# Kernel optimization log

Measured on AMD Instinct MI355X. Metric: run time of the kernel, lower is better.

The kernel has to match this reference:

```python
import jax, jax.numpy as jnp
import numpy as np

N_NODES = 50000
N_EDGES = 800000
D_IN = 128
D_OUT = 128
N_MLP = 2


def _lin(x, W, b):
    return x @ W.T + b


def setup_inputs() -> dict:
    key = jax.random.key(0)
    ks = jax.random.split(key, 32)
    d = {}
    d['feat'] = jax.random.normal(ks[0], (N_NODES, D_IN), dtype=jnp.float32)
    d['src'] = jax.random.randint(ks[1], (N_EDGES,), 0, N_NODES, dtype=jnp.int32)
    d['dst'] = jax.random.randint(ks[2], (N_EDGES,), 0, N_NODES, dtype=jnp.int32)
    s_in = 1.0 / np.sqrt(D_IN)
    s_out = 1.0 / np.sqrt(D_OUT)
    i = 3
    def w(shape, s):
        nonlocal i
        out = jax.random.normal(ks[i], shape, dtype=jnp.float32) * s
        i += 1
        return out
    for nm in ['asrc', 'adst', 'asub', 'amul']:
        d['W_' + nm] = w((D_OUT, D_IN), s_in)
        d['b_' + nm] = w((D_OUT,), s_in)
    d['W_aout'] = w((1, D_OUT), s_out)
    d['b_aout'] = w((1,), s_out)
    for nm in ['pool', 'pool2']:
        d['W_' + nm] = w((D_IN, D_IN), s_in)
        d['b_' + nm] = w((D_IN,), s_in)
    for nm in ['self', 'neigh', 'neigh2']:
        d['W_' + nm] = w((D_OUT, D_IN), s_in)
        d['b_' + nm] = w((D_OUT,), s_in)
    d['W_mlp'] = w((N_MLP, D_OUT, D_OUT), s_out)
    d['b_mlp'] = w((N_MLP, D_OUT), s_out)
    return d


def reference(feat, src, dst,
              W_asrc, b_asrc, W_adst, b_adst, W_asub, b_asub, W_amul, b_amul,
              W_aout, b_aout, W_pool, b_pool, W_pool2, b_pool2,
              W_self, b_self, W_neigh, b_neigh, W_neigh2, b_neigh2,
              W_mlp, b_mlp):
    gelu = lambda x: jax.nn.gelu(x, approximate=False)
    fs = feat[src]            # [E, D_IN] gathered source feats
    fd = feat[dst]            # [E, D_IN] gathered dest feats
    # edge attention score
    e = _lin(fs - fd, W_asub, b_asub) + _lin(fs * fd, W_amul, b_amul)
    e = e + _lin(feat, W_asrc, b_asrc)[src] + _lin(feat, W_adst, b_adst)[dst]
    e = gelu(e)
    e = jax.nn.leaky_relu(_lin(e, W_aout, b_aout), 0.2)  # [E, 1]
    deg = jax.ops.segment_sum(jnp.ones((src.shape[0],), jnp.float32), dst,
                              num_segments=N_NODES)      # in-degree
    has_in = (deg > 0)[:, None]
    # max-pool branch
    h = gelu(_lin(feat, W_pool, b_pool))
    m = e * h[src]
    neigh = jax.ops.segment_max(m, dst, num_segments=N_NODES)
    neigh = jnp.where(has_in, neigh, 0.0)
    # mean-pool branch
    h2 = gelu(_lin(feat, W_pool2, b_pool2))
    m2 = e * h2[src]
    neigh2 = jax.ops.segment_sum(m2, dst, num_segments=N_NODES)
    neigh2 = neigh2 / jnp.maximum(deg, 1.0)[:, None]
    rst = _lin(feat, W_self, b_self) + _lin(neigh, W_neigh, b_neigh) \
        + _lin(neigh2, W_neigh2, b_neigh2)
    for li in range(W_mlp.shape[0]):
        rst = rst + _lin(gelu(rst), W_mlp[li], b_mlp[li])
    return rst
```

## Files before the change

kernel.cpp:

```cpp
#include <hip/hip_runtime.h>
#include <cstdint>
#include <cstddef>

#define NN 50000
#define NE 800000
#define DD 128

static_assert(NN % 16 == 0, "node tiles");
static_assert(NE % 16 == 0, "edge tiles");

typedef __bf16 bf16_t;
typedef bf16_t bf16x8 __attribute__((ext_vector_type(8)));
typedef bf16_t bf16x4 __attribute__((ext_vector_type(4)));
typedef bf16_t bf16x2 __attribute__((ext_vector_type(2)));
typedef float f32x4 __attribute__((ext_vector_type(4)));
typedef float f32x16 __attribute__((ext_vector_type(16)));

__device__ __forceinline__ float gelu_f(float x) {
    float u = x * x;
    float t = fmaf(u, -0.1029442445f, -2.3021184019f);
    float s = __builtin_amdgcn_exp2f(x * t);
    return x * __builtin_amdgcn_rcpf(1.0f + s);
}

__device__ __forceinline__ int frag_idx(int ch, int k) {
    int t = ch >> 4, n = ch & 15;
    int kb = k >> 5, r = k & 31, q = r >> 3, j = r & 7;
    return ((((t * 4 + kb) * 4 + q) * 16 + n) << 3) + j;
}

__device__ __forceinline__ int frag32_idx(int ch, int k) {
    int t = ch >> 5, m = ch & 31;
    int kc = k >> 4, q = (k >> 3) & 1, j = k & 7;
    return ((((t * 8 + kc) * 2 + q) * 32 + m) << 3) + j;
}

__global__ __launch_bounds__(256) void convert_feat_kernel(
    const float* __restrict__ feat, bf16_t* __restrict__ fb,
    const int* __restrict__ dst, int* __restrict__ deg)
{
    int i = blockIdx.x * 256 + threadIdx.x;
    f32x4 v = ((const f32x4*)feat)[i];
    bf16x4 o;
    o[0] = (bf16_t)v[0]; o[1] = (bf16_t)v[1]; o[2] = (bf16_t)v[2]; o[3] = (bf16_t)v[3];
    ((bf16x4*)fb)[i] = o;
    if (i < NE) atomicAdd(&deg[dst[i]], 1);
}

__global__ __launch_bounds__(256) void prep_kernel(
    const float* __restrict__ W_asrc, const float* __restrict__ b_asrc,
    const float* __restrict__ W_adst, const float* __restrict__ b_adst,
    const float* __restrict__ W_asub, const float* __restrict__ b_asub,
    const float* __restrict__ W_amul, const float* __restrict__ b_amul,
    const float* __restrict__ W_pool, const float* __restrict__ W_pool2,
    const float* __restrict__ W_self, const float* __restrict__ b_self,
    const float* __restrict__ W_neigh, const float* __restrict__ b_neigh,
    const float* __restrict__ W_neigh2, const float* __restrict__ b_neigh2,
    const float* __restrict__ W_mlp,
    bf16_t* __restrict__ W_Sf, bf16_t* __restrict__ W_Df, bf16_t* __restrict__ W_amulf,
    bf16_t* __restrict__ W_poolf, bf16_t* __restrict__ W_pool2f,
    bf16_t* __restrict__ W_selff, bf16_t* __restrict__ W_neighf, bf16_t* __restrict__ W_neigh2f,
    bf16_t* __restrict__ W_mlpf,
    float* __restrict__ b_e, float* __restrict__ b_rst)
{
    int gid = blockIdx.x * 256 + threadIdx.x;
    float sub = W_asub[gid];
    int ch = gid >> 7, k = gid & 127;
    int fi = frag_idx(ch, k);
    W_Sf[fi] = (bf16_t)(W_asrc[gid] + sub);
    W_Df[fi] = (bf16_t)(W_adst[gid] - sub);
    W_amulf[frag32_idx(ch, k)] = (bf16_t)W_amul[gid];
    W_poolf[fi]   = (bf16_t)W_pool[gid];
    W_pool2f[fi]  = (bf16_t)W_pool2[gid];
    W_selff[fi]   = (bf16_t)W_self[gid];
    W_neighf[fi]  = (bf16_t)W_neigh[gid];
    W_neigh2f[fi] = (bf16_t)W_neigh2[gid];
    W_mlpf[fi]            = (bf16_t)W_mlp[gid];
    W_mlpf[DD * DD + fi]  = (bf16_t)W_mlp[DD * DD + gid];
    if (gid < DD) {
        b_e[gid]   = b_asub[gid] + b_amul[gid] + b_asrc[gid] + b_adst[gid];
        b_rst[gid] = b_self[gid] + b_neigh[gid] + b_neigh2[gid];
    }
}

__device__ __forceinline__ void mm16_store_ilv(
    const bf16x8 a[4], const bf16_t* __restrict__ Wf, const float* __restrict__ bias,
    bf16_t* __restrict__ hh, int nb, int n, int q, int lane, int sub)
{
#pragma unroll
    for (int t = 0; t < 8; t++) {
        f32x4 acc = {0.f, 0.f, 0.f, 0.f};
#pragma unroll
        for (int kb = 0; kb < 4; kb++) {
            bf16x8 b = *(const bf16x8*)(Wf + (((t * 4 + kb) * 64 + lane) << 3));
            acc = __builtin_amdgcn_mfma_f32_16x16x32_bf16(a[kb], b, acc, 0, 0, 0);
        }
        int ch = t * 16 + n;
        int pos = ((ch >> 1) << 2) + (ch & 1) + sub;
        float bv = bias[ch];
#pragma unroll
        for (int r = 0; r < 4; r++)
            hh[(size_t)(nb + q * 4 + r) * 256 + pos] = (bf16_t)gelu_f(acc[r] + bv);
    }
}

__device__ __forceinline__ void mm16_store_plain(
    const bf16x8 a[4], const bf16_t* __restrict__ Wf, const float* __restrict__ bias,
    bf16_t* __restrict__ out, int nb, int n, int q, int lane)
{
#pragma unroll
    for (int t = 0; t < 8; t++) {
        f32x4 acc = {0.f, 0.f, 0.f, 0.f};
#pragma unroll
        for (int kb = 0; kb < 4; kb++) {
            bf16x8 b = *(const bf16x8*)(Wf + (((t * 4 + kb) * 64 + lane) << 3));
            acc = __builtin_amdgcn_mfma_f32_16x16x32_bf16(a[kb], b, acc, 0, 0, 0);
        }
        int ch = t * 16 + n;
        float bv = bias ? bias[ch] : 0.0f;
#pragma unroll
        for (int r = 0; r < 4; r++)
            out[(size_t)(nb + q * 4 + r) * DD + ch] = (bf16_t)(acc[r] + bv);
    }
}

__global__ __launch_bounds__(256) void node_linear_kernel(
    const bf16_t* __restrict__ fb,
    const bf16_t* __restrict__ W_poolf, const float* __restrict__ b_pool,
    const bf16_t* __restrict__ W_pool2f, const float* __restrict__ b_pool2,
    const bf16_t* __restrict__ W_Sf, const float* __restrict__ b_e,
    const bf16_t* __restrict__ W_Df,
    const int* __restrict__ src, const int* __restrict__ dst,
    int* __restrict__ cursor, int2* __restrict__ csr,
    bf16_t* __restrict__ hh, bf16_t* __restrict__ us, bf16_t* __restrict__ ud)
{
    int gtid = blockIdx.x * 256 + threadIdx.x;
    if (gtid < NE / 4) {
        int4 s4 = ((const int4*)src)[gtid];
        int4 d4 = ((const int4*)dst)[gtid];
#pragma unroll
        for (int j = 0; j < 4; j++) {
            int d = (&d4.x)[j];
            int pos = atomicAdd(&cursor[d << 4], 1);
            int2 pk;
            pk.x = (&s4.x)[j];
            pk.y = d;
            csr[pos] = pk;
        }
    }

    int wid = blockIdx.x * 4 + (threadIdx.x >> 6);
    if (wid >= NN / 16) return;
    int lane = threadIdx.x & 63, n = lane & 15, q = lane >> 4;
    int nb = wid * 16;
    bf16x8 a[4];
#pragma unroll
    for (int kb = 0; kb < 4; kb++)
        a[kb] = *(const bf16x8*)(fb + (size_t)(nb + n) * DD + kb * 32 + q * 8);
    mm16_store_ilv(a, W_poolf, b_pool, hh, nb, n, q, lane, 0);
    mm16_store_ilv(a, W_pool2f, b_pool2, hh, nb, n, q, lane, 2);
    mm16_store_plain(a, W_Sf, b_e, us, nb, n, q, lane);
    mm16_store_plain(a, W_Df, nullptr, ud, nb, n, q, lane);
}

#define SCAN_NB ((NN + 255) / 256)

__global__ __launch_bounds__(256) void scan1_kernel(const int* __restrict__ deg,
                                                    int* __restrict__ offsets, int* __restrict__ bsum)
{
    __shared__ int tmp[256];
    int t = threadIdx.x, g = blockIdx.x * 256 + t;
    int v = (g < NN) ? deg[g] : 0;
    tmp[t] = v;
    __syncthreads();
#pragma unroll
    for (int d = 1; d < 256; d <<= 1) {
        int x = (t >= d) ? tmp[t - d] : 0;
        __syncthreads();
        tmp[t] += x;
        __syncthreads();
    }
    if (g < NN) offsets[g] = tmp[t] - v;
    if (t == 255) bsum[blockIdx.x] = tmp[255];
}

__global__ __launch_bounds__(256) void scan2_kernel(const int* __restrict__ bsum, int* __restrict__ bbase)
{
    __shared__ int tmp[256];
    int t = threadIdx.x;
    int v = (t < SCAN_NB) ? bsum[t] : 0;
    tmp[t] = v;
    __syncthreads();
#pragma unroll
    for (int d = 1; d < 256; d <<= 1) {
        int x = (t >= d) ? tmp[t - d] : 0;
        __syncthreads();
        tmp[t] += x;
        __syncthreads();
    }
    if (t < SCAN_NB) bbase[t] = tmp[t] - v;
}

__global__ __launch_bounds__(256) void scan3_kernel(const int* __restrict__ bbase,
                                                    int* __restrict__ offsets, int* __restrict__ cursor)
{
    int g = blockIdx.x * 256 + threadIdx.x;
    if (g < NN) {
        int o = offsets[g] + bbase[blockIdx.x];
        offsets[g] = o;
        cursor[g << 4] = o;
    }
}

#define ES_NBLK 2500
#define ES_ITERS (NE / 32 / ES_NBLK)

__global__ __launch_bounds__(256, 4) void edge_score_kernel(
    const bf16_t* __restrict__ fb,
    const bf16_t* __restrict__ us, const bf16_t* __restrict__ ud,
    const bf16_t* __restrict__ W_amulf,
    const float* __restrict__ w_aout, const float* __restrict__ b_aout,
    int2* __restrict__ csr)
{
    __shared__ __align__(16) bf16_t sP[2][32 * 128];
    __shared__ __align__(16) bf16_t sU[2][32 * 128];
    __shared__ float partials[32 * 5];
    __shared__ float sWa[128];
    int tid = threadIdx.x;
    int wave = tid >> 6, lane = tid & 63;
    int n = lane & 31, q = lane >> 5;
    int t = wave;

    if (tid < 128) sWa[tid] = w_aout[tid];

    bf16x8 wAm[8];
#pragma unroll
    for (int kc = 0; kc < 8; kc++)
        wAm[kc] = *(const bf16x8*)(W_amulf + ((((t * 8 + kc) * 2 + q) * 32 + n) << 3));
    float bout = b_aout[0];

    int sed0 = tid >> 4, sc = tid & 15;

    int e0 = blockIdx.x * 32;
    int2 pk0 = csr[e0 + sed0];
    int2 pk1 = csr[e0 + sed0 + 16];
    bf16x8 pfs0 = *(const bf16x8*)(fb + (size_t)pk0.x * DD + sc * 8);
    bf16x8 pfd0 = *(const bf16x8*)(fb + (size_t)pk0.y * DD + sc * 8);
    bf16x8 pus0 = *(const bf16x8*)(us + (size_t)pk0.x * DD + sc * 8);
    bf16x8 pud0 = *(const bf16x8*)(ud + (size_t)pk0.y * DD + sc * 8);
    bf16x8 pfs1 = *(const bf16x8*)(fb + (size_t)pk1.x * DD + sc * 8);
    bf16x8 pfd1 = *(const bf16x8*)(fb + (size_t)pk1.y * DD + sc * 8);
    bf16x8 pus1 = *(const bf16x8*)(us + (size_t)pk1.x * DD + sc * 8);
    bf16x8 pud1 = *(const bf16x8*)(ud + (size_t)pk1.y * DD + sc * 8);

    for (int it = 0; it < ES_ITERS; it++) {
        int buf = it & 1;
        int eb = (blockIdx.x + it * ES_NBLK) * 32;
        {
            bf16x8 pp, uu;
#pragma unroll
            for (int j = 0; j < 8; j++) {
                pp[j] = (bf16_t)((float)pfs0[j] * (float)pfd0[j]);
                uu[j] = (bf16_t)((float)pus0[j] + (float)pud0[j]);
            }
            int ph = (sc ^ (sed0 & 7)) << 3;
            *(bf16x8*)(sP[buf] + sed0 * 128 + ph) = pp;
            *(bf16x8*)(sU[buf] + sed0 * 128 + ph) = uu;
        }
        {
            int ed = sed0 + 16;
            bf16x8 pp, uu;
#pragma unroll
            for (int j = 0; j < 8; j++) {
                pp[j] = (bf16_t)((float)pfs1[j] * (float)pfd1[j]);
                uu[j] = (bf16_t)((float)pus1[j] + (float)pud1[j]);
            }
            int ph = (sc ^ (ed & 7)) << 3;
            *(bf16x8*)(sP[buf] + ed * 128 + ph) = pp;
            *(bf16x8*)(sU[buf] + ed * 128 + ph) = uu;
        }
        __syncthreads();
        if (it + 1 < ES_ITERS) {
            int e1 = (blockIdx.x + (it + 1) * ES_NBLK) * 32;
            pk0 = csr[e1 + sed0];
            pk1 = csr[e1 + sed0 + 16];
            pfs0 = *(const bf16x8*)(fb + (size_t)pk0.x * DD + sc * 8);
            pfd0 = *(const bf16x8*)(fb + (size_t)pk0.y * DD + sc * 8);
            pus0 = *(const bf16x8*)(us + (size_t)pk0.x * DD + sc * 8);
            pud0 = *(const bf16x8*)(ud + (size_t)pk0.y * DD + sc * 8);
            pfs1 = *(const bf16x8*)(fb + (size_t)pk1.x * DD + sc * 8);
            pfd1 = *(const bf16x8*)(fb + (size_t)pk1.y * DD + sc * 8);
            pus1 = *(const bf16x8*)(us + (size_t)pk1.x * DD + sc * 8);
            pud1 = *(const bf16x8*)(ud + (size_t)pk1.y * DD + sc * 8);
        }
        f32x16 acc = {};
        int swz = n & 7;
#pragma unroll
        for (int kc = 0; kc < 8; kc++) {
            bf16x8 bP = *(const bf16x8*)(sP[buf] + n * 128 + (((kc * 2 + q) ^ swz) << 3));
            acc = __builtin_amdgcn_mfma_f32_32x32x16_bf16(wAm[kc], bP, acc, 0, 0, 0);
        }
        float psum = 0.f;
#pragma unroll
        for (int c = 0; c < 4; c++) {
            bf16x4 sv = *(const bf16x4*)(sU[buf] + n * 128 + (((t * 4 + c) ^ swz) << 3) + q * 4);
            f32x4 wv = *(const f32x4*)(sWa + t * 32 + c * 8 + q * 4);
#pragma unroll
            for (int j = 0; j < 4; j++)
                psum = fmaf(gelu_f(acc[c * 4 + j] + (float)sv[j]), wv[j], psum);
        }
        psum += __shfl_xor(psum, 32, 64);
        if (lane < 32) partials[lane * 5 + wave] = psum;
        __syncthreads();
        if (wave == (it & 3) && lane < 32) {
            const float* pr = partials + lane * 5;
            float s = pr[0] + pr[1] + pr[2] + pr[3] + bout;
            s = s > 0.f ? s : 0.2f * s;
            csr[eb + lane].y = __float_as_int(s);
        }
    }
}

__global__ __launch_bounds__(256) void aggregate_kernel(
    const bf16_t* __restrict__ hh,
    const int* __restrict__ offsets, const int* __restrict__ deg,
    const int2* __restrict__ csr,
    bf16_t* __restrict__ neigh, bf16_t* __restrict__ neigh2)
{
    int wave = threadIdx.x >> 6, lane = threadIdx.x & 63;
    int v = blockIdx.x * 4 + wave;
    if (v >= NN) return;
    int off = offsets[v];
    int dg = deg[v];
    int quarter = lane >> 4;
    int cl = lane & 15;
    float mx[8], sm[8];
#pragma unroll
    for (int j = 0; j < 8; j++) { mx[j] = -INFINITY; sm[j] = 0.f; }
    for (int base = 0; base < dg; base += 64) {
        int cnt = dg - base; if (cnt > 64) cnt = 64;
        int s_l = 0; float sc_l = 0.f;
        if (lane < cnt) {
            int2 pk = csr[off + base + lane];
            s_l = pk.x;
            sc_l = __int_as_float(pk.y);
        }
        int nit = (cnt + 3) >> 2;
#pragma unroll 2
        for (int i = 0; i < nit; i++) {
            int idx = 4 * i + quarter;
            int s = __shfl(s_l, idx, 64);
            float sc = __shfl(sc_l, idx, 64);
            if (idx < cnt) {
                const bf16_t* row = hh + (size_t)s * 256 + 16 * cl;
                bf16x8 h0 = *(const bf16x8*)(row);
                bf16x8 h1 = *(const bf16x8*)(row + 8);
                mx[0] = fmaxf(mx[0], sc * (float)h0[0]);
                mx[1] = fmaxf(mx[1], sc * (float)h0[1]);
                sm[0] = fmaf(sc, (float)h0[2], sm[0]);
                sm[1] = fmaf(sc, (float)h0[3], sm[1]);
                mx[2] = fmaxf(mx[2], sc * (float)h0[4]);
                mx[3] = fmaxf(mx[3], sc * (float)h0[5]);
                sm[2] = fmaf(sc, (float)h0[6], sm[2]);
                sm[3] = fmaf(sc, (float)h0[7], sm[3]);
                mx[4] = fmaxf(mx[4], sc * (float)h1[0]);
                mx[5] = fmaxf(mx[5], sc * (float)h1[1]);
                sm[4] = fmaf(sc, (float)h1[2], sm[4]);
                sm[5] = fmaf(sc, (float)h1[3], sm[5]);
                mx[6] = fmaxf(mx[6], sc * (float)h1[4]);
                mx[7] = fmaxf(mx[7], sc * (float)h1[5]);
                sm[6] = fmaf(sc, (float)h1[6], sm[6]);
                sm[7] = fmaf(sc, (float)h1[7], sm[7]);
            }
        }
    }
#pragma unroll
    for (int j = 0; j < 8; j++) {
        mx[j] = fmaxf(mx[j], __shfl_xor(mx[j], 16, 64));
        mx[j] = fmaxf(mx[j], __shfl_xor(mx[j], 32, 64));
        sm[j] += __shfl_xor(sm[j], 16, 64);
        sm[j] += __shfl_xor(sm[j], 32, 64);
    }
    if (quarter == 0) {
        float inv = 1.0f / (float)(dg > 1 ? dg : 1);
        bf16x8 n1, n2;
#pragma unroll
        for (int j = 0; j < 8; j++) {
            n1[j] = (bf16_t)(dg > 0 ? mx[j] : 0.0f);
            n2[j] = (bf16_t)(sm[j] * inv);
        }
        *(bf16x8*)(neigh + (size_t)v * DD + 8 * cl) = n1;
        *(bf16x8*)(neigh2 + (size_t)v * DD + 8 * cl) = n2;
    }
}

__global__ __launch_bounds__(256) void final_kernel(
    const bf16_t* __restrict__ fb, const bf16_t* __restrict__ neigh, const bf16_t* __restrict__ neigh2,
    const bf16_t* __restrict__ W_selff, const bf16_t* __restrict__ W_neighf, const bf16_t* __restrict__ W_neigh2f,
    const float* __restrict__ b_rst,
    const bf16_t* __restrict__ W_mlpf, const float* __restrict__ b_mlp,
    float* __restrict__ out)
{
    __shared__ __align__(16) float lds[4][16 * 132];
    int wave = threadIdx.x >> 6;
    int wid = blockIdx.x * 4 + wave;
    if (wid >= NN / 16) return;
    int lane = threadIdx.x & 63, n = lane & 15, q = lane >> 4;
    int nb = wid * 16;
    float* L = lds[wave];

    bf16x8 af[4], an[4], am[4];
#pragma unroll
    for (int kb = 0; kb < 4; kb++) {
        size_t o = (size_t)(nb + n) * DD + kb * 32 + q * 8;
        af[kb] = *(const bf16x8*)(fb + o);
        an[kb] = *(const bf16x8*)(neigh + o);
        am[kb] = *(const bf16x8*)(neigh2 + o);
    }
    f32x4 rst[8];
#pragma unroll
    for (int t = 0; t < 8; t++) {
        f32x4 acc = {0.f, 0.f, 0.f, 0.f};
#pragma unroll
        for (int kb = 0; kb < 4; kb++) {
            int wo = ((t * 4 + kb) * 64 + lane) << 3;
            acc = __builtin_amdgcn_mfma_f32_16x16x32_bf16(af[kb], *(const bf16x8*)(W_selff + wo), acc, 0, 0, 0);
            acc = __builtin_amdgcn_mfma_f32_16x16x32_bf16(an[kb], *(const bf16x8*)(W_neighf + wo), acc, 0, 0, 0);
            acc = __builtin_amdgcn_mfma_f32_16x16x32_bf16(am[kb], *(const bf16x8*)(W_neigh2f + wo), acc, 0, 0, 0);
        }
        float bv = b_rst[t * 16 + n];
#pragma unroll
        for (int r = 0; r < 4; r++) acc[r] += bv;
        rst[t] = acc;
    }

#pragma unroll
    for (int li = 0; li < 2; li++) {
#pragma unroll
        for (int t = 0; t < 8; t++)
#pragma unroll
            for (int r = 0; r < 4; r++)
                L[(q * 4 + r) * 132 + t * 16 + n] = gelu_f(rst[t][r]);
        __builtin_amdgcn_wave_barrier();
        bf16x8 g[4];
#pragma unroll
        for (int kb = 0; kb < 4; kb++) {
            const f32x4* p = (const f32x4*)&L[n * 132 + kb * 32 + q * 8];
            f32x4 x0 = p[0], x1 = p[1];
            bf16x8 gg;
            gg[0] = (bf16_t)x0[0]; gg[1] = (bf16_t)x0[1]; gg[2] = (bf16_t)x0[2]; gg[3] = (bf16_t)x0[3];
            gg[4] = (bf16_t)x1[0]; gg[5] = (bf16_t)x1[1]; gg[6] = (bf16_t)x1[2]; gg[7] = (bf16_t)x1[3];
            g[kb] = gg;
        }
        __builtin_amdgcn_wave_barrier();
        const bf16_t* Wl = W_mlpf + li * DD * DD;
#pragma unroll
        for (int t = 0; t < 8; t++) {
            f32x4 acc = {0.f, 0.f, 0.f, 0.f};
#pragma unroll
            for (int kb = 0; kb < 4; kb++) {
                bf16x8 b = *(const bf16x8*)(Wl + (((t * 4 + kb) * 64 + lane) << 3));
                acc = __builtin_amdgcn_mfma_f32_16x16x32_bf16(g[kb], b, acc, 0, 0, 0);
            }
            float bm = b_mlp[li * DD + t * 16 + n];
#pragma unroll
            for (int r = 0; r < 4; r++) rst[t][r] += acc[r] + bm;
        }
    }

#pragma unroll
    for (int t = 0; t < 8; t++)
#pragma unroll
        for (int r = 0; r < 4; r++)
            out[(size_t)(nb + q * 4 + r) * DD + t * 16 + n] = rst[t][r];
}

extern "C" void kernel_launch(void* const* d_in, const int* in_sizes, int n_in,
                              void* d_out, int out_size, void* d_ws, size_t ws_size,
                              hipStream_t stream)
{
    const float* feat    = (const float*)d_in[0];
    const int*   src     = (const int*)d_in[1];
    const int*   dst     = (const int*)d_in[2];
    const float* W_asrc  = (const float*)d_in[3],  *b_asrc  = (const float*)d_in[4];
    const float* W_adst  = (const float*)d_in[5],  *b_adst  = (const float*)d_in[6];
    const float* W_asub  = (const float*)d_in[7],  *b_asub  = (const float*)d_in[8];
    const float* W_amul  = (const float*)d_in[9],  *b_amul  = (const float*)d_in[10];
    const float* W_aout  = (const float*)d_in[11], *b_aout  = (const float*)d_in[12];
    const float* W_pool  = (const float*)d_in[13], *b_pool  = (const float*)d_in[14];
    const float* W_pool2 = (const float*)d_in[15], *b_pool2 = (const float*)d_in[16];
    const float* W_self  = (const float*)d_in[17], *b_self  = (const float*)d_in[18];
    const float* W_neigh = (const float*)d_in[19], *b_neigh = (const float*)d_in[20];
    const float* W_neigh2= (const float*)d_in[21], *b_neigh2= (const float*)d_in[22];
    const float* W_mlp   = (const float*)d_in[23], *b_mlp   = (const float*)d_in[24];
    float* out = (float*)d_out;

    char* w = (char*)d_ws;
    auto take = [&](size_t bytes) -> void* {
        void* p = (void*)w;
        w += (bytes + 255) & ~(size_t)255;
        return p;
    };
    bf16_t* fb      = (bf16_t*)take((size_t)NN * DD * sizeof(bf16_t));
    bf16_t* neigh   = (bf16_t*)take((size_t)NN * DD * sizeof(bf16_t));
    bf16_t* neigh2  = (bf16_t*)take((size_t)NN * DD * sizeof(bf16_t));
    bf16_t* hh      = (bf16_t*)take((size_t)NN * 256 * sizeof(bf16_t));
    bf16_t* us      = (bf16_t*)take((size_t)NN * DD * sizeof(bf16_t));
    bf16_t* ud      = (bf16_t*)take((size_t)NN * DD * sizeof(bf16_t));
    int*    deg     = (int*)take((size_t)NN * sizeof(int));
    int*    offsets = (int*)take((size_t)NN * sizeof(int));
    int*    cursor  = (int*)take((size_t)NN * 16 * sizeof(int));
    int2*   csr     = (int2*)take((size_t)NE * sizeof(int2));
    int*    bsum    = (int*)take(256 * sizeof(int));
    int*    bbase   = (int*)take(256 * sizeof(int));
    bf16_t* W_Sf    = (bf16_t*)take((size_t)DD * DD * sizeof(bf16_t));
    bf16_t* W_Df    = (bf16_t*)take((size_t)DD * DD * sizeof(bf16_t));
    bf16_t* W_amulf = (bf16_t*)take((size_t)DD * DD * sizeof(bf16_t));
    bf16_t* W_poolf = (bf16_t*)take((size_t)DD * DD * sizeof(bf16_t));
    bf16_t* W_pool2f= (bf16_t*)take((size_t)DD * DD * sizeof(bf16_t));
    bf16_t* W_selff = (bf16_t*)take((size_t)DD * DD * sizeof(bf16_t));
    bf16_t* W_neighf= (bf16_t*)take((size_t)DD * DD * sizeof(bf16_t));
    bf16_t* W_neigh2f=(bf16_t*)take((size_t)DD * DD * sizeof(bf16_t));
    bf16_t* W_mlpf  = (bf16_t*)take((size_t)2 * DD * DD * sizeof(bf16_t));
    float*  b_e     = (float*)take((size_t)DD * sizeof(float));
    float*  b_rst   = (float*)take((size_t)DD * sizeof(float));

    (void)hipMemsetAsync(deg, 0, (size_t)NN * sizeof(int), stream);

    convert_feat_kernel<<<NN * DD / 4 / 256, 256, 0, stream>>>(feat, fb, dst, deg);

    prep_kernel<<<DD * DD / 256, 256, 0, stream>>>(
        W_asrc, b_asrc, W_adst, b_adst, W_asub, b_asub, W_amul, b_amul,
        W_pool, W_pool2, W_self, b_self, W_neigh, b_neigh, W_neigh2, b_neigh2, W_mlp,
        W_Sf, W_Df, W_amulf, W_poolf, W_pool2f, W_selff, W_neighf, W_neigh2f, W_mlpf,
        b_e, b_rst);

    scan1_kernel<<<SCAN_NB, 256, 0, stream>>>(deg, offsets, bsum);
    scan2_kernel<<<1, 256, 0, stream>>>(bsum, bbase);
    scan3_kernel<<<SCAN_NB, 256, 0, stream>>>(bbase, offsets, cursor);

    const int nwaves = NN / 16;
    const int ngrid = (nwaves + 3) / 4;
    node_linear_kernel<<<ngrid, 256, 0, stream>>>(
        fb, W_poolf, b_pool, W_pool2f, b_pool2, W_Sf, b_e, W_Df,
        src, dst, cursor, csr, hh, us, ud);

    edge_score_kernel<<<ES_NBLK, 256, 0, stream>>>(
        fb, us, ud, W_amulf, W_aout, b_aout, csr);

    aggregate_kernel<<<(NN + 3) / 4, 256, 0, stream>>>(
        hh, offsets, deg, csr, neigh, neigh2);

    final_kernel<<<ngrid, 256, 0, stream>>>(
        fb, neigh, neigh2, W_selff, W_neighf, W_neigh2f, b_rst, W_mlpf, b_mlp, out);
}
```

Measured before the change: 429.0 us.

## Build CSR via two-level bucket sort instead of global atomic degree scan

Replaces the global per-node atomic degree count, three-kernel scan and atomic cursor scatter with a bucketed counting sort. Edges are first scattered into 391 fixed-size buckets of 128 destination nodes using LDS histograms and one global atomic per bucket per block. A per-bucket kernel then computes local degrees, offsets and the final CSR placement in shared memory. This cuts contention on global atomics and scattered writes, at the cost of an extra pass over the edges and a fixed bucket capacity of 4096 that could overflow on skewed degree distributions.

```diff
diff --git a/kernel.cpp b/kernel.cpp
--- a/kernel.cpp
+++ b/kernel.cpp
@@ -6,13 +6,16 @@
 #define NE 800000
 #define DD 128
 
+#define NBK 391
+#define BSLOT 4096
+
 static_assert(NN % 16 == 0, "node tiles");
 static_assert(NE % 16 == 0, "edge tiles");
+static_assert(((NN + 127) >> 7) == NBK, "bucket count");
 
 typedef __bf16 bf16_t;
 typedef bf16_t bf16x8 __attribute__((ext_vector_type(8)));
 typedef bf16_t bf16x4 __attribute__((ext_vector_type(4)));
-typedef bf16_t bf16x2 __attribute__((ext_vector_type(2)));
 typedef float f32x4 __attribute__((ext_vector_type(4)));
 typedef float f32x16 __attribute__((ext_vector_type(16)));
 
@@ -36,15 +39,13 @@
 }
 
 __global__ __launch_bounds__(256) void convert_feat_kernel(
-    const float* __restrict__ feat, bf16_t* __restrict__ fb,
-    const int* __restrict__ dst, int* __restrict__ deg)
+    const float* __restrict__ feat, bf16_t* __restrict__ fb)
 {
     int i = blockIdx.x * 256 + threadIdx.x;
     f32x4 v = ((const f32x4*)feat)[i];
     bf16x4 o;
     o[0] = (bf16_t)v[0]; o[1] = (bf16_t)v[1]; o[2] = (bf16_t)v[2]; o[3] = (bf16_t)v[3];
     ((bf16x4*)fb)[i] = o;
-    if (i < NE) atomicAdd(&deg[dst[i]], 1);
 }
 
 __global__ __launch_bounds__(256) void prep_kernel(
@@ -83,6 +84,114 @@
     }
 }
 
+__global__ __launch_bounds__(256) void scatter_bucket_kernel(
+    const int* __restrict__ src, const int* __restrict__ dst,
+    int* __restrict__ gcursor, int2* __restrict__ ebuf)
+{
+    __shared__ int cnt[NBK];
+    __shared__ int ofs[NBK];
+    int t = threadIdx.x;
+    for (int b = t; b < NBK; b += 256) cnt[b] = 0;
+    __syncthreads();
+    int qbase = blockIdx.x * 1024 + t;
+    int4 s4[4], d4[4];
+    bool valid[4];
+#pragma unroll
+    for (int k = 0; k < 4; k++) {
+        int q = qbase + k * 256;
+        valid[k] = q < NE / 4;
+        if (valid[k]) {
+            s4[k] = ((const int4*)src)[q];
+            d4[k] = ((const int4*)dst)[q];
+#pragma unroll
+            for (int j = 0; j < 4; j++)
+                atomicAdd(&cnt[((&d4[k].x)[j]) >> 7], 1);
+        }
+    }
+    __syncthreads();
+    for (int b = t; b < NBK; b += 256) {
+        int c = cnt[b];
+        ofs[b] = c ? atomicAdd(&gcursor[b], c) : 0;
+    }
+    __syncthreads();
+#pragma unroll
+    for (int k = 0; k < 4; k++) {
+        if (valid[k]) {
+#pragma unroll
+            for (int j = 0; j < 4; j++) {
+                int d = (&d4[k].x)[j];
+                int b = d >> 7;
+                int p = atomicAdd(&ofs[b], 1);
+                int2 pk;
+                pk.x = (&s4[k].x)[j];
+                pk.y = d;
+                ebuf[(size_t)b * BSLOT + p] = pk;
+            }
+        }
+    }
+}
+
+__global__ __launch_bounds__(512) void bucket_scan_kernel(
+    const int* __restrict__ gcursor, int* __restrict__ boff)
+{
+    __shared__ int tmp[512];
+    int t = threadIdx.x;
+    int v = (t < NBK) ? gcursor[t] : 0;
+    tmp[t] = v;
+    __syncthreads();
+#pragma unroll
+    for (int d = 1; d < 512; d <<= 1) {
+        int x = (t >= d) ? tmp[t - d] : 0;
+        __syncthreads();
+        tmp[t] += x;
+        __syncthreads();
+    }
+    if (t < NBK) boff[t] = tmp[t] - v;
+}
+
+__global__ __launch_bounds__(256) void finalize_csr_kernel(
+    const int2* __restrict__ ebuf, const int* __restrict__ gcursor, const int* __restrict__ boff,
+    int2* __restrict__ csr, int* __restrict__ offsets, int* __restrict__ deg)
+{
+    __shared__ int lcnt[128];
+    __shared__ int nbase[128];
+    __shared__ int pre[128];
+    int B = blockIdx.x, t = threadIdx.x;
+    int v0 = B << 7;
+    int cnt = gcursor[B];
+    int dbase = boff[B];
+    const int2* eb = ebuf + (size_t)B * BSLOT;
+    if (t < 128) lcnt[t] = 0;
+    __syncthreads();
+    for (int i = t; i < cnt; i += 256)
+        atomicAdd(&lcnt[eb[i].y - v0], 1);
+    __syncthreads();
+    int c = (t < 128) ? lcnt[t] : 0;
+    if (t < 128) pre[t] = c;
+    __syncthreads();
+#pragma unroll
+    for (int d = 1; d < 128; d <<= 1) {
+        int x = (t >= d && t < 128) ? pre[t - d] : 0;
+        __syncthreads();
+        if (t < 128) pre[t] += x;
+        __syncthreads();
+    }
+    if (t < 128) {
+        int nb = dbase + pre[t] - c;
+        nbase[t] = nb;
+        int v = v0 + t;
+        if (v < NN) { offsets[v] = nb; deg[v] = c; }
+        lcnt[t] = 0;
+    }
+    __syncthreads();
+    for (int i = t; i < cnt; i += 256) {
+        int2 pk = eb[i];
+        int j = pk.y - v0;
+        int pos = nbase[j] + atomicAdd(&lcnt[j], 1);
+        csr[pos] = pk;
+    }
+}
+
 __device__ __forceinline__ void mm16_store_ilv(
     const bf16x8 a[4], const bf16_t* __restrict__ Wf, const float* __restrict__ bias,
     bf16_t* __restrict__ hh, int nb, int n, int q, int lane, int sub)
@@ -130,25 +239,8 @@
     const bf16_t* __restrict__ W_pool2f, const float* __restrict__ b_pool2,
     const bf16_t* __restrict__ W_Sf, const float* __restrict__ b_e,
     const bf16_t* __restrict__ W_Df,
-    const int* __restrict__ src, const int* __restrict__ dst,
-    int* __restrict__ cursor, int2* __restrict__ csr,
     bf16_t* __restrict__ hh, bf16_t* __restrict__ us, bf16_t* __restrict__ ud)
 {
-    int gtid = blockIdx.x * 256 + threadIdx.x;
-    if (gtid < NE / 4) {
-        int4 s4 = ((const int4*)src)[gtid];
-        int4 d4 = ((const int4*)dst)[gtid];
-#pragma unroll
-        for (int j = 0; j < 4; j++) {
-            int d = (&d4.x)[j];
-            int pos = atomicAdd(&cursor[d << 4], 1);
-            int2 pk;
-            pk.x = (&s4.x)[j];
-            pk.y = d;
-            csr[pos] = pk;
-        }
-    }
-
     int wid = blockIdx.x * 4 + (threadIdx.x >> 6);
     if (wid >= NN / 16) return;
     int lane = threadIdx.x & 63, n = lane & 15, q = lane >> 4;
@@ -161,55 +253,6 @@
     mm16_store_ilv(a, W_pool2f, b_pool2, hh, nb, n, q, lane, 2);
     mm16_store_plain(a, W_Sf, b_e, us, nb, n, q, lane);
     mm16_store_plain(a, W_Df, nullptr, ud, nb, n, q, lane);
-}
-
-#define SCAN_NB ((NN + 255) / 256)
-
-__global__ __launch_bounds__(256) void scan1_kernel(const int* __restrict__ deg,
-                                                    int* __restrict__ offsets, int* __restrict__ bsum)
-{
-    __shared__ int tmp[256];
-    int t = threadIdx.x, g = blockIdx.x * 256 + t;
-    int v = (g < NN) ? deg[g] : 0;
-    tmp[t] = v;
-    __syncthreads();
-#pragma unroll
-    for (int d = 1; d < 256; d <<= 1) {
-        int x = (t >= d) ? tmp[t - d] : 0;
-        __syncthreads();
-        tmp[t] += x;
-        __syncthreads();
-    }
-    if (g < NN) offsets[g] = tmp[t] - v;
-    if (t == 255) bsum[blockIdx.x] = tmp[255];
-}
-
-__global__ __launch_bounds__(256) void scan2_kernel(const int* __restrict__ bsum, int* __restrict__ bbase)
-{
-    __shared__ int tmp[256];
-    int t = threadIdx.x;
-    int v = (t < SCAN_NB) ? bsum[t] : 0;
-    tmp[t] = v;
-    __syncthreads();
-#pragma unroll
-    for (int d = 1; d < 256; d <<= 1) {
-        int x = (t >= d) ? tmp[t - d] : 0;
-        __syncthreads();
-        tmp[t] += x;
-        __syncthreads();
-    }
-    if (t < SCAN_NB) bbase[t] = tmp[t] - v;
-}
-
-__global__ __launch_bounds__(256) void scan3_kernel(const int* __restrict__ bbase,
-                                                    int* __restrict__ offsets, int* __restrict__ cursor)
-{
-    int g = blockIdx.x * 256 + threadIdx.x;
-    if (g < NN) {
-        int o = offsets[g] + bbase[blockIdx.x];
-        offsets[g] = o;
-        cursor[g << 4] = o;
-    }
 }
 
 #define ES_NBLK 2500
@@ -509,10 +552,10 @@
     bf16_t* ud      = (bf16_t*)take((size_t)NN * DD * sizeof(bf16_t));
     int*    deg     = (int*)take((size_t)NN * sizeof(int));
     int*    offsets = (int*)take((size_t)NN * sizeof(int));
-    int*    cursor  = (int*)take((size_t)NN * 16 * sizeof(int));
     int2*   csr     = (int2*)take((size_t)NE * sizeof(int2));
-    int*    bsum    = (int*)take(256 * sizeof(int));
-    int*    bbase   = (int*)take(256 * sizeof(int));
+    int2*   ebuf    = (int2*)take((size_t)NBK * BSLOT * sizeof(int2));
+    int*    gcursor = (int*)take((size_t)NBK * sizeof(int));
+    int*    boff    = (int*)take((size_t)NBK * sizeof(int));
     bf16_t* W_Sf    = (bf16_t*)take((size_t)DD * DD * sizeof(bf16_t));
     bf16_t* W_Df    = (bf16_t*)take((size_t)DD * DD * sizeof(bf16_t));
     bf16_t* W_amulf = (bf16_t*)take((size_t)DD * DD * sizeof(bf16_t));
@@ -525,9 +568,9 @@
     float*  b_e     = (float*)take((size_t)DD * sizeof(float));
     float*  b_rst   = (float*)take((size_t)DD * sizeof(float));
 
-    (void)hipMemsetAsync(deg, 0, (size_t)NN * sizeof(int), stream);
-
-    convert_feat_kernel<<<NN * DD / 4 / 256, 256, 0, stream>>>(feat, fb, dst, deg);
+    (void)hipMemsetAsync(gcursor, 0, (size_t)NBK * sizeof(int), stream);
+
+    convert_feat_kernel<<<NN * DD / 4 / 256, 256, 0, stream>>>(feat, fb);
 
     prep_kernel<<<DD * DD / 256, 256, 0, stream>>>(
         W_asrc, b_asrc, W_adst, b_adst, W_asub, b_asub, W_amul, b_amul,
@@ -535,15 +578,14 @@
         W_Sf, W_Df, W_amulf, W_poolf, W_pool2f, W_selff, W_neighf, W_neigh2f, W_mlpf,
         b_e, b_rst);
 
-    scan1_kernel<<<SCAN_NB, 256, 0, stream>>>(deg, offsets, bsum);
-    scan2_kernel<<<1, 256, 0, stream>>>(bsum, bbase);
-    scan3_kernel<<<SCAN_NB, 256, 0, stream>>>(bbase, offsets, cursor);
+    scatter_bucket_kernel<<<(NE / 4 + 1023) / 1024, 256, 0, stream>>>(src, dst, gcursor, ebuf);
+    bucket_scan_kernel<<<1, 512, 0, stream>>>(gcursor, boff);
+    finalize_csr_kernel<<<NBK, 256, 0, stream>>>(ebuf, gcursor, boff, csr, offsets, deg);
 
     const int nwaves = NN / 16;
     const int ngrid = (nwaves + 3) / 4;
     node_linear_kernel<<<ngrid, 256, 0, stream>>>(
-        fb, W_poolf, b_pool, W_pool2f, b_pool2, W_Sf, b_e, W_Df,
-        src, dst, cursor, csr, hh, us, ud);
+        fb, W_poolf, b_pool, W_pool2f, b_pool2, W_Sf, b_e, W_Df, hh, us, ud);
 
     edge_score_kernel<<<ES_NBLK, 256, 0, stream>>>(
         fb, us, ud, W_amulf, W_aout, b_aout, csr);
```

Result: faster. 359.2 us (-16.3%).
